# Kernel optimization log

Measured on AMD Instinct MI355X. Metric: run time of the kernel, lower is better.

## Reference

```python
import jax, jax.numpy as jnp
import numpy as np

N = 10000
E = 80000
NUM_TYPES = 1000
IN_CH = 64
EMB = 128
IN_GNN = EMB + IN_CH - 1  # 191
NUM_GRAPHS = 16
NUM_CLASSES = 2


def _glorot(key, shape):
    fan_in, fan_out = shape[0], shape[1]
    lim = jnp.sqrt(6.0 / (fan_in + fan_out))
    return jax.random.uniform(key, shape, jnp.float32, -lim, lim)


def setup_inputs() -> dict:
    key = jax.random.key(0)
    ks = jax.random.split(key, 20)
    node_type_ids = jax.random.randint(ks[0], (N,), 0, NUM_TYPES)
    other_feats = jax.random.normal(ks[1], (N, IN_CH - 1), jnp.float32)
    edge_index = jax.random.randint(ks[2], (2, E), 0, N)
    batch = jnp.sort(jax.random.randint(ks[3], (N,), 0, NUM_GRAPHS))
    params = dict(
        emb=jax.random.normal(ks[4], (NUM_TYPES, EMB), jnp.float32),
        W1=_glorot(ks[5], (IN_GNN, 2048)), b1=jnp.zeros((2048,), jnp.float32),
        W2=_glorot(ks[6], (2048, 1024)), b2=jnp.zeros((1024,), jnp.float32),
        W3=_glorot(ks[7], (1024, 1024)), b3=jnp.zeros((1024,), jnp.float32),
        h1w=_glorot(ks[8], (1024, 1024)), h1b=jnp.zeros((1024,), jnp.float32),
        h2w=_glorot(ks[9], (1024, 1024)), h2b=jnp.zeros((1024,), jnp.float32),
        h3w=_glorot(ks[10], (1024, 512)), h3b=jnp.zeros((512,), jnp.float32),
        ow=_glorot(ks[11], (512, NUM_CLASSES)), ob=jnp.zeros((NUM_CLASSES,), jnp.float32),
    )
    return dict(node_type_ids=node_type_ids, other_feats=other_feats,
                edge_index=edge_index, batch=batch, **params)


def _gcn_norm(edge_index, num_nodes):
    # add self loops + symmetric normalization D^-1/2 (A+I) D^-1/2 (PyG GCNConv defaults)
    loop = jnp.arange(num_nodes, dtype=edge_index.dtype)
    src = jnp.concatenate([edge_index[0], loop])
    dst = jnp.concatenate([edge_index[1], loop])
    deg = jax.ops.segment_sum(jnp.ones_like(src, jnp.float32), dst, num_segments=num_nodes)
    dinv = jnp.where(deg > 0, jax.lax.rsqrt(jnp.maximum(deg, 1.0)), 0.0)
    norm = dinv[src] * dinv[dst]
    return src, dst, norm


def _gcn_conv(x, src, dst, norm, W, b):
    h = x @ W                                    # [N, out] dense GEMM first (PyG order)
    msg = h[src] * norm[:, None]                 # gather + scale over edges
    agg = jax.ops.segment_sum(msg, dst, num_segments=x.shape[0])  # scatter-add
    return agg + b


def reference(node_type_ids, other_feats, edge_index, batch,
              emb, W1, b1, W2, b2, W3, b3,
              h1w, h1b, h2w, h2b, h3w, h3b, ow, ob):
    # eval mode: dropout is identity
    x = jnp.concatenate([emb[node_type_ids], other_feats], axis=-1)  # [N, 191]
    src, dst, norm = _gcn_norm(edge_index, x.shape[0])
    x = jax.nn.relu(_gcn_conv(x, src, dst, norm, W1, b1))
    x = jax.nn.relu(_gcn_conv(x, src, dst, norm, W2, b2))
    x = jax.nn.relu(_gcn_conv(x, src, dst, norm, W3, b3))
    # global mean pool over graphs
    sums = jax.ops.segment_sum(x, batch, num_segments=NUM_GRAPHS)
    cnts = jax.ops.segment_sum(jnp.ones((x.shape[0],), jnp.float32), batch, num_segments=NUM_GRAPHS)
    g = sums / jnp.maximum(cnts, 1.0)[:, None]   # [G, 1024]
    g = jax.nn.relu(g @ h1w + h1b)
    g = jax.nn.relu(g @ h2w + h2b)
    g = jax.nn.relu(g @ h3w + h3b)
    return g @ ow + ob                           # [G, num_classes]
```

## Files before the change

### kernel.cpp

```cpp
#include <hip/hip_runtime.h>


#define N_NODES 10000
#define N_EDGES 80000
#define EMB_DIM 128
#define FEAT_DIM 63
#define IN_GNN 191
#define IN_STRIDE 192
#define H1 2048
#define H2 1024
#define NGRAPH 16
#define NCLS 2
#define PCHUNK 8

#define GLB_AS __attribute__((address_space(1)))
#define LDS_AS __attribute__((address_space(3)))

using ushort = unsigned short;
typedef __attribute__((ext_vector_type(8))) short s8b;
typedef __attribute__((ext_vector_type(4))) float f4v;

__device__ __forceinline__ float us2f(ushort u) {
    union { unsigned int i; float f; } v; v.i = ((unsigned int)u) << 16; return v.f;
}
__device__ __forceinline__ ushort f2us(float f) {
    union { unsigned int i; float f; } v; v.f = f;
    unsigned int r = v.i + 0x7FFFu + ((v.i >> 16) & 1u);
    return (ushort)(r >> 16);
}
__device__ __forceinline__ float ldm(const void* p, long i, int md) {
    return (md == 1) ? us2f(((const ushort*)p)[i]) : ((const float*)p)[i];
}
__device__ __forceinline__ void gl_lds16(const ushort* g, ushort* l) {
    __builtin_amdgcn_global_load_lds((const GLB_AS unsigned int*)g,
                                     (LDS_AS unsigned int*)l, 16, 0, 0);
}

__global__ void GraphV1EmbLarge_73864847556672_kernel() {}

__global__ void k_detect(const ushort* __restrict__ feats, int* __restrict__ mode) {
    if (threadIdx.x != 0 || blockIdx.x != 0) return;
    int sane = 0;
    for (int i = 0; i < 256; i++) {
        ushort u = feats[i];
        int e = (u >> 7) & 0xFF;
        if (u == 0 || (e >= 97 && e <= 157)) sane++;
    }
    *mode = (sane >= 220) ? 1 : 2;
}

__global__ void k_zero2(int* __restrict__ a, int na, float* __restrict__ b, int nb) {
    int i = blockIdx.x * 256 + threadIdx.x;
    if (i < na) a[i] = 0;
    if (i < nb) b[i] = 0.f;
}
__global__ void k_deg_i(const int* __restrict__ dst, int* __restrict__ cnt) {
    int e = blockIdx.x * blockDim.x + threadIdx.x;
    if (e < N_EDGES) atomicAdd(&cnt[dst[e]], 1);
}
__global__ void k_dinv_i(const int* __restrict__ cnt, float* __restrict__ dinv) {
    int i = blockIdx.x * blockDim.x + threadIdx.x;
    if (i < N_NODES) dinv[i] = rsqrtf((float)cnt[i] + 1.0f);
}
__global__ void k_scan(const int* __restrict__ cnt, int* __restrict__ indptr) {
    __shared__ int part[256];
    int t = threadIdx.x;
    int base = t * 40;
    int s = 0;
    for (int i = 0; i < 40; i++) { int idx = base + i; if (idx < N_NODES) s += cnt[idx]; }
    part[t] = s;
    __syncthreads();
    if (t == 0) {
        int run = 0;
        for (int i = 0; i < 256; i++) { int tmp = part[i]; part[i] = run; run += tmp; }
        indptr[N_NODES] = run;
    }
    __syncthreads();
    int run = part[t];
    for (int i = 0; i < 40; i++) {
        int idx = base + i;
        if (idx < N_NODES) { indptr[idx] = run; run += cnt[idx]; }
    }
}
__global__ void k_fill(const int* __restrict__ src, const int* __restrict__ dst,
                       const int* __restrict__ indptr, int* __restrict__ cursor,
                       const float* __restrict__ dinv, int* __restrict__ ecol,
                       float* __restrict__ ewgt) {
    int e = blockIdx.x * blockDim.x + threadIdx.x;
    if (e >= N_EDGES) return;
    int d = dst[e], s = src[e];
    int slot = indptr[d] + atomicAdd(&cursor[d], 1);
    ecol[slot] = s;
    ewgt[slot] = dinv[s] * dinv[d];
}
__global__ void k_starts(const int* __restrict__ batch, int* __restrict__ starts) {
    int i = blockIdx.x * blockDim.x + threadIdx.x;
    if (i > N_NODES) return;
    int bc = (i < N_NODES) ? batch[i] : NGRAPH;
    int bp = (i == 0) ? -1 : batch[i - 1];
    for (int g = bp + 1; g <= bc; g++) starts[g] = i;
}

__global__ void k_build_x0(const int* __restrict__ types, const void* __restrict__ emb,
                           const void* __restrict__ feats, ushort* __restrict__ x0,
                           const int* __restrict__ mode) {
    int md = *mode;
    int i = blockIdx.x;
    int c = threadIdx.x;
    float v = 0.f;
    if (c < EMB_DIM) v = ldm(emb, (long)types[i] * EMB_DIM + c, md);
    else if (c < IN_GNN) v = ldm(feats, (long)i * FEAT_DIM + (c - EMB_DIM), md);
    x0[(long)i * IN_STRIDE + c] = f2us(v);
}

__global__ void k_cvtT(const void* __restrict__ W, int K, int N, int Kp,
                       ushort* __restrict__ Wt, const int* __restrict__ mode) {
    __shared__ float tile[32][33];
    int md = *mode;
    int n0 = blockIdx.x * 32, k0 = blockIdx.y * 32;
    int tx = threadIdx.x, ty = threadIdx.y;
    for (int r = ty; r < 32; r += 8) {
        int k = k0 + r;
        tile[r][tx] = (k < K) ? ldm(W, (long)k * N + n0 + tx, md) : 0.f;
    }
    __syncthreads();
    for (int r = ty; r < 32; r += 8) {
        int nn = n0 + r, kk = k0 + tx;
        if (kk < Kp) Wt[(long)nn * Kp + kk] = f2us(tile[tx][r]);
    }
}

__global__ void k_biases(const void* __restrict__ b1, const void* __restrict__ b2,
                         const void* __restrict__ b3, float* __restrict__ b1f,
                         float* __restrict__ b2f, float* __restrict__ b3f,
                         const int* __restrict__ mode) {
    int md = *mode;
    int i = blockIdx.x * 256 + threadIdx.x;
    if (i < 2048) b1f[i] = ldm(b1, i, md);
    else if (i < 3072) b2f[i - 2048] = ldm(b2, (long)(i - 2048), md);
    else if (i < 4096) b3f[i - 3072] = ldm(b3, (long)(i - 3072), md);
}

__global__ void k_gather192(const ushort* __restrict__ H, const int* __restrict__ indptr,
                            const int* __restrict__ ecol, const float* __restrict__ ewgt,
                            const float* __restrict__ dinv, ushort* __restrict__ X) {
    int d = blockIdx.x;
    int c = threadIdx.x;
    float ds = dinv[d];
    float acc = us2f(H[(long)d * IN_STRIDE + c]) * ds * ds;
    int s0 = indptr[d], s1 = indptr[d + 1];
    for (int s = s0; s < s1; s++) {
        int sc = ecol[s];
        float w = ewgt[s];
        acc += us2f(H[(long)sc * IN_STRIDE + c]) * w;
    }
    X[(long)d * IN_STRIDE + c] = f2us(acc);
}

__device__ __forceinline__ void unpack8(uint4 u, float* f) {
    f[0] = us2f((ushort)(u.x & 0xffff)); f[1] = us2f((ushort)(u.x >> 16));
    f[2] = us2f((ushort)(u.y & 0xffff)); f[3] = us2f((ushort)(u.y >> 16));
    f[4] = us2f((ushort)(u.z & 0xffff)); f[5] = us2f((ushort)(u.z >> 16));
    f[6] = us2f((ushort)(u.w & 0xffff)); f[7] = us2f((ushort)(u.w >> 16));
}

__global__ void k_gather1024(const ushort* __restrict__ H, const int* __restrict__ indptr,
                             const int* __restrict__ ecol, const float* __restrict__ ewgt,
                             const float* __restrict__ dinv, const float* __restrict__ bias,
                             ushort* __restrict__ X) {
    int d = blockIdx.x;
    int c8 = threadIdx.x * 8;
    float ds = dinv[d];
    float a[8], f[8];
    unpack8(*(const uint4*)&H[(long)d * H2 + c8], a);
    float w0 = ds * ds;
#pragma unroll
    for (int r = 0; r < 8; r++) a[r] *= w0;
    int s0 = indptr[d], s1 = indptr[d + 1];
    for (int s = s0; s < s1; s++) {
        int sc = ecol[s];
        float w = ewgt[s];
        unpack8(*(const uint4*)&H[(long)sc * H2 + c8], f);
#pragma unroll
        for (int r = 0; r < 8; r++) a[r] += f[r] * w;
    }
    uint4 o;
    unsigned int p0 = (unsigned int)f2us(fmaxf(a[0] + bias[c8 + 0], 0.f));
    unsigned int p1 = (unsigned int)f2us(fmaxf(a[1] + bias[c8 + 1], 0.f));
    unsigned int p2 = (unsigned int)f2us(fmaxf(a[2] + bias[c8 + 2], 0.f));
    unsigned int p3 = (unsigned int)f2us(fmaxf(a[3] + bias[c8 + 3], 0.f));
    unsigned int p4 = (unsigned int)f2us(fmaxf(a[4] + bias[c8 + 4], 0.f));
    unsigned int p5 = (unsigned int)f2us(fmaxf(a[5] + bias[c8 + 5], 0.f));
    unsigned int p6 = (unsigned int)f2us(fmaxf(a[6] + bias[c8 + 6], 0.f));
    unsigned int p7 = (unsigned int)f2us(fmaxf(a[7] + bias[c8 + 7], 0.f));
    o.x = p0 | (p1 << 16); o.y = p2 | (p3 << 16);
    o.z = p4 | (p5 << 16); o.w = p6 | (p7 << 16);
    *(uint4*)&X[(long)d * H2 + c8] = o;
}

__global__ __launch_bounds__(256) void k_mfma_gemm(
    const ushort* __restrict__ A, int lda, int M,
    const ushort* __restrict__ Wt, int K, int N,
    const float* __restrict__ bias, int relu,
    ushort* __restrict__ C) {
    __shared__ ushort As[128 * 32];
    __shared__ ushort Bs[128 * 32];
    int n0 = blockIdx.x * 128, m0 = blockIdx.y * 128;
    int tid = threadIdx.x;
    int wave = tid >> 6, lane = tid & 63;
    int wm = (wave & 1) * 64, wn = (wave >> 1) * 64;
    int quad = lane >> 4, l16 = lane & 15;

    int rr = lane >> 2;
    int cc = (lane & 3) * 8;
    int rA0 = wave * 16 + rr, rA1 = 64 + rA0;
    int gmA0 = m0 + rA0; if (gmA0 >= M) gmA0 = M - 1;
    int gmA1 = m0 + rA1; if (gmA1 >= M) gmA1 = M - 1;
    const ushort* aS0 = A + (long)gmA0 * lda + cc;
    const ushort* aS1 = A + (long)gmA1 * lda + cc;
    const ushort* bS0 = Wt + (long)(n0 + rA0) * K + cc;
    const ushort* bS1 = Wt + (long)(n0 + rA1) * K + cc;
    ushort* aD0 = As + wave * 512;
    ushort* aD1 = As + 2048 + wave * 512;
    ushort* bD0 = Bs + wave * 512;
    ushort* bD1 = Bs + 2048 + wave * 512;

    f4v acc[4][4];
#pragma unroll
    for (int i = 0; i < 4; i++)
#pragma unroll
        for (int j = 0; j < 4; j++) acc[i][j] = (f4v)(0.f);

    for (int k0 = 0; k0 < K; k0 += 32) {
        gl_lds16(aS0, aD0);
        gl_lds16(aS1, aD1);
        gl_lds16(bS0, bD0);
        gl_lds16(bS1, bD1);
        aS0 += 32; aS1 += 32; bS0 += 32; bS1 += 32;
        __syncthreads();
        s8b a[4], b[4];
#pragma unroll
        for (int i = 0; i < 4; i++)
            a[i] = *(const s8b*)&As[(wm + i * 16 + l16) * 32 + quad * 8];
#pragma unroll
        for (int j = 0; j < 4; j++)
            b[j] = *(const s8b*)&Bs[(wn + j * 16 + l16) * 32 + quad * 8];
#pragma unroll
        for (int i = 0; i < 4; i++)
#pragma unroll
            for (int j = 0; j < 4; j++)
                acc[i][j] = __builtin_amdgcn_mfma_f32_16x16x32_bf16(a[i], b[j], acc[i][j], 0, 0, 0);
        __syncthreads();
    }

#pragma unroll
    for (int i = 0; i < 4; i++) {
        int row0 = m0 + wm + i * 16 + quad * 4;
#pragma unroll
        for (int j = 0; j < 4; j++) {
            int colc = n0 + wn + j * 16 + l16;
            float bv = bias ? bias[colc] : 0.f;
#pragma unroll
            for (int r = 0; r < 4; r++) {
                int row = row0 + r;
                if (row < M) {
                    float v = acc[i][j][r] + bv;
                    if (relu) v = fmaxf(v, 0.f);
                    C[(long)row * N + colc] = f2us(v);
                }
            }
        }
    }
}

__global__ void k_pool_part(const ushort* __restrict__ x, const int* __restrict__ starts,
                            float* __restrict__ acc) {
    int g = blockIdx.x / PCHUNK, ch = blockIdx.x % PCHUNK;
    int c = blockIdx.y * 256 + threadIdx.x;
    int s0 = starts[g], s1 = starts[g + 1];
    int len = s1 - s0;
    int per = (len + PCHUNK - 1) / PCHUNK;
    int r0 = s0 + ch * per;
    int r1 = r0 + per; if (r1 > s1) r1 = s1;
    if (r0 >= r1) return;
    float sum = 0.f;
    for (int i = r0; i < r1; i++) sum += us2f(x[(long)i * H2 + c]);
    atomicAdd(&acc[g * H2 + c], sum);
}
__global__ void k_pool_fin(const float* __restrict__ acc, const int* __restrict__ starts,
                           ushort* __restrict__ pA) {
    int idx = blockIdx.x * 256 + threadIdx.x;
    if (idx >= NGRAPH * H2) return;
    int g = idx >> 10;
    int cnt = starts[g + 1] - starts[g];
    pA[idx] = f2us(acc[idx] / (float)(cnt > 0 ? cnt : 1));
}

__global__ __launch_bounds__(256) void k_head_mfma(const ushort* __restrict__ A,
                                                   const ushort* __restrict__ Wt,
                                                   float* __restrict__ pt, int N) {
    __shared__ float red[4][16][16];
    int n0 = blockIdx.x * 16;
    int ks = blockIdx.y;
    int wave = threadIdx.x >> 6, lane = threadIdx.x & 63;
    int l16 = lane & 15, quad = lane >> 4;
    int kbase = ks * 256 + wave * 64;
    f4v acc = (f4v)(0.f);
#pragma unroll
    for (int kk = 0; kk < 64; kk += 32) {
        int k = kbase + kk + quad * 8;
        s8b a = *(const s8b*)&A[l16 * 1024 + k];
        s8b b = *(const s8b*)&Wt[(long)(n0 + l16) * 1024 + k];
        acc = __builtin_amdgcn_mfma_f32_16x16x32_bf16(a, b, acc, 0, 0, 0);
    }
#pragma unroll
    for (int r = 0; r < 4; r++) red[wave][quad * 4 + r][l16] = acc[r];
    __syncthreads();
    int row = threadIdx.x >> 4, col = threadIdx.x & 15;
    float s = red[0][row][col] + red[1][row][col] + red[2][row][col] + red[3][row][col];
    pt[((long)ks * 16 + row) * N + n0 + col] = s;
}

__global__ void k_head_red(const float* __restrict__ pt, const void* __restrict__ bias,
                           ushort* __restrict__ out, int N,
                           const int* __restrict__ mode) {
    int md = *mode;
    int idx = blockIdx.x * 256 + threadIdx.x;
    if (idx >= 16 * N) return;
    int row = idx / N, col = idx - row * N;
    float s = pt[((long)0 * 16 + row) * N + col] + pt[((long)1 * 16 + row) * N + col]
            + pt[((long)2 * 16 + row) * N + col] + pt[((long)3 * 16 + row) * N + col];
    s = fmaxf(s + ldm(bias, (long)col, md), 0.f);
    out[(long)row * N + col] = f2us(s);
}

__global__ void k_head_out(const ushort* __restrict__ in, const void* __restrict__ W,
                           const void* __restrict__ b, void* __restrict__ out,
                           const int* __restrict__ mode) {
    int md = *mode;
    int row = blockIdx.x >> 1, cls = blockIdx.x & 1;
    int lane = threadIdx.x;
    float acc = 0.f;
    for (int k = lane; k < 512; k += 64)
        acc += us2f(in[row * 512 + k]) * ldm(W, (long)k * NCLS + cls, md);
#pragma unroll
    for (int off = 32; off > 0; off >>= 1) acc += __shfl_down(acc, off);
    if (lane == 0) {
        float v = acc + ldm(b, (long)cls, md);
        if (md == 1) ((ushort*)out)[row * NCLS + cls] = f2us(v);
        else ((float*)out)[row * NCLS + cls] = v;
    }
}

extern "C" void kernel_launch(void* const* d_in, const int* in_sizes, int n_in,
                              void* d_out, int out_size, void* d_ws, size_t ws_size,
                              hipStream_t stream) {
    static const int EXPECT[19] = {
        10000, 630000, 160000, 10000, 128000,
        391168, 2048, 2097152, 1024, 1048576, 1024,
        1048576, 1024, 1048576, 1024, 524288, 512, 1024, 2
    };
    if (n_in != 19) { hipMemsetAsync(d_out, 0x48, 64, stream); return; }
    for (int i = 0; i < 19; i++)
        if (in_sizes[i] != EXPECT[i]) { hipMemsetAsync(d_out, 0x50 + i, 64, stream); return; }
    if (ws_size < (size_t)90000000) { hipMemsetAsync(d_out, 0x49, 64, stream); return; }

    const int* node_types = (const int*)d_in[0];
    const void* other = d_in[1];
    const int* e_src = (const int*)d_in[2];
    const int* e_dst = e_src + N_EDGES;
    const int* batch = (const int*)d_in[3];

    char* w = (char*)d_ws;
    int* mode = (int*)w;      w += 256;
    int* cnt = (int*)w;       w += 10240 * 4;
    int* cursor = (int*)w;    w += 10240 * 4;
    float* dinv = (float*)w;  w += 10240 * 4;
    int* starts = (int*)w;    w += 256;
    int* indptr = (int*)w;    w += 10240 * 4;
    int* ecol = (int*)w;      w += 81920 * 4;
    float* ewgt = (float*)w;  w += 81920 * 4;
    float* b1f = (float*)w;   w += 2048 * 4;
    float* b2f = (float*)w;   w += 1024 * 4;
    float* b3f = (float*)w;   w += 1024 * 4;
    float* pt = (float*)w;    w += 4 * 16 * 1024 * 4;
    float* pacc = (float*)w;  w += 16 * 1024 * 4;
    ushort* pA = (ushort*)w;  w += 16 * 1024 * 2;
    ushort* hA = (ushort*)w;  w += 16 * 1024 * 2;
    ushort* hB = (ushort*)w;  w += 16 * 1024 * 2;
    ushort* x0 = (ushort*)w;  w += 1920000 * 2;
    ushort* A1 = (ushort*)w;  w += 1920000 * 2;
    ushort* W1t = (ushort*)w; w += 393216 * 2;
    ushort* W2t = (ushort*)w; w += 2097152 * 2;
    ushort* W3t = (ushort*)w; w += 1048576 * 2;
    ushort* h1wt = (ushort*)w; w += 1048576 * 2;
    ushort* h2wt = (ushort*)w; w += 1048576 * 2;
    ushort* h3wt = (ushort*)w; w += 524288 * 2;
    ushort* Hb = (ushort*)w;  w += 20480000 * 2;
    ushort* Gb = (ushort*)w;  w += 10240000 * 2;
    ushort* x2 = Hb;
    ushort* x3 = Hb + (size_t)N_NODES * H2;

    hipGetLastError();
    k_detect<<<1, 64, 0, stream>>>((const ushort*)other, mode);
    hipError_t e0 = hipGetLastError();
    if (e0 != hipSuccess) { hipMemsetAsync(d_out, 0x46, 64, stream); return; }

    k_zero2<<<80, 256, 0, stream>>>(cnt, 20480, pacc, NGRAPH * H2);
    k_deg_i<<<(N_EDGES + 255) / 256, 256, 0, stream>>>(e_dst, cnt);
    k_dinv_i<<<(N_NODES + 255) / 256, 256, 0, stream>>>(cnt, dinv);
    k_starts<<<(N_NODES + 256) / 256, 256, 0, stream>>>(batch, starts);
    k_scan<<<1, 256, 0, stream>>>(cnt, indptr);
    k_fill<<<(N_EDGES + 255) / 256, 256, 0, stream>>>(e_src, e_dst, indptr, cursor, dinv, ecol, ewgt);

    k_build_x0<<<N_NODES, IN_STRIDE, 0, stream>>>(node_types, d_in[4], other, x0, mode);
    k_cvtT<<<dim3(H1 / 32, IN_STRIDE / 32), dim3(32, 8), 0, stream>>>(d_in[5], IN_GNN, H1, IN_STRIDE, W1t, mode);
    k_cvtT<<<dim3(H2 / 32, H1 / 32), dim3(32, 8), 0, stream>>>(d_in[7], H1, H2, H1, W2t, mode);
    k_cvtT<<<dim3(H2 / 32, H2 / 32), dim3(32, 8), 0, stream>>>(d_in[9], H2, H2, H2, W3t, mode);
    k_cvtT<<<dim3(H2 / 32, H2 / 32), dim3(32, 8), 0, stream>>>(d_in[11], H2, H2, H2, h1wt, mode);
    k_cvtT<<<dim3(H2 / 32, H2 / 32), dim3(32, 8), 0, stream>>>(d_in[13], H2, H2, H2, h2wt, mode);
    k_cvtT<<<dim3(512 / 32, H2 / 32), dim3(32, 8), 0, stream>>>(d_in[15], H2, 512, H2, h3wt, mode);
    k_biases<<<16, 256, 0, stream>>>(d_in[6], d_in[8], d_in[10], b1f, b2f, b3f, mode);

    const int MB = (N_NODES + 127) / 128;

    k_gather192<<<N_NODES, IN_STRIDE, 0, stream>>>(x0, indptr, ecol, ewgt, dinv, A1);
    k_mfma_gemm<<<dim3(H1 / 128, MB), 256, 0, stream>>>(A1, IN_STRIDE, N_NODES, W1t, IN_STRIDE, H1, b1f, 1, Hb);

    k_mfma_gemm<<<dim3(H2 / 128, MB), 256, 0, stream>>>(Hb, H1, N_NODES, W2t, H1, H2, nullptr, 0, Gb);
    k_gather1024<<<N_NODES, 128, 0, stream>>>(Gb, indptr, ecol, ewgt, dinv, b2f, x2);

    k_mfma_gemm<<<dim3(H2 / 128, MB), 256, 0, stream>>>(x2, H2, N_NODES, W3t, H2, H2, nullptr, 0, Gb);
    k_gather1024<<<N_NODES, 128, 0, stream>>>(Gb, indptr, ecol, ewgt, dinv, b3f, x3);

    k_pool_part<<<dim3(NGRAPH * PCHUNK, H2 / 256), 256, 0, stream>>>(x3, starts, pacc);
    k_pool_fin<<<64, 256, 0, stream>>>(pacc, starts, pA);

    k_head_mfma<<<dim3(64, 4), 256, 0, stream>>>(pA, h1wt, pt, 1024);
    k_head_red<<<64, 256, 0, stream>>>(pt, d_in[12], hA, 1024, mode);
    k_head_mfma<<<dim3(64, 4), 256, 0, stream>>>(hA, h2wt, pt, 1024);
    k_head_red<<<64, 256, 0, stream>>>(pt, d_in[14], hB, 1024, mode);
    k_head_mfma<<<dim3(32, 4), 256, 0, stream>>>(hB, h3wt, pt, 512);
    k_head_red<<<32, 256, 0, stream>>>(pt, d_in[16], hA, 512, mode);
    k_head_out<<<NGRAPH * NCLS, 64, 0, stream>>>(hA, d_in[17], d_in[18], d_out, mode);

    hipError_t e1 = hipGetLastError();
    if (e1 != hipSuccess) hipMemsetAsync(d_out, 0x47, 64, stream);
}
```

Measured before the change: 451.4 us.

## Rework GEMM staging with padded LDS, grouped tile order, and fused prep kernels

Replaces the direct global-to-LDS loads in the MFMA GEMM with register-staged vector loads into padded LDS tiles (row pitch 40) to reduce bank conflicts. The grid becomes 1D with a grouped M/N tile swizzle so that eight M-tiles share weight tiles for better L2 reuse. It also folds the dinv computation into the scan kernel and merges the six weight transpose-convert launches into one kernel, cutting launch overhead. The register-staged path adds a global-load latency stall before each barrier, since there is no double buffering.

```diff
diff --git a/kernel.cpp b/kernel.cpp
--- a/kernel.cpp
+++ b/kernel.cpp
@@ -12,9 +12,7 @@
 #define NGRAPH 16
 #define NCLS 2
 #define PCHUNK 8
-
-#define GLB_AS __attribute__((address_space(1)))
-#define LDS_AS __attribute__((address_space(3)))
+#define LDP 40
 
 using ushort = unsigned short;
 typedef __attribute__((ext_vector_type(8))) short s8b;
@@ -30,10 +28,6 @@
 }
 __device__ __forceinline__ float ldm(const void* p, long i, int md) {
     return (md == 1) ? us2f(((const ushort*)p)[i]) : ((const float*)p)[i];
-}
-__device__ __forceinline__ void gl_lds16(const ushort* g, ushort* l) {
-    __builtin_amdgcn_global_load_lds((const GLB_AS unsigned int*)g,
-                                     (LDS_AS unsigned int*)l, 16, 0, 0);
 }
 
 __global__ void GraphV1EmbLarge_73864847556672_kernel() {}
@@ -58,11 +52,8 @@
     int e = blockIdx.x * blockDim.x + threadIdx.x;
     if (e < N_EDGES) atomicAdd(&cnt[dst[e]], 1);
 }
-__global__ void k_dinv_i(const int* __restrict__ cnt, float* __restrict__ dinv) {
-    int i = blockIdx.x * blockDim.x + threadIdx.x;
-    if (i < N_NODES) dinv[i] = rsqrtf((float)cnt[i] + 1.0f);
-}
-__global__ void k_scan(const int* __restrict__ cnt, int* __restrict__ indptr) {
+__global__ void k_scan(const int* __restrict__ cnt, int* __restrict__ indptr,
+                       float* __restrict__ dinv) {
     __shared__ int part[256];
     int t = threadIdx.x;
     int base = t * 40;
@@ -79,7 +70,10 @@
     int run = part[t];
     for (int i = 0; i < 40; i++) {
         int idx = base + i;
-        if (idx < N_NODES) { indptr[idx] = run; run += cnt[idx]; }
+        if (idx < N_NODES) {
+            indptr[idx] = run; run += cnt[idx];
+            dinv[idx] = rsqrtf((float)cnt[idx] + 1.0f);
+        }
     }
 }
 __global__ void k_fill(const int* __restrict__ src, const int* __restrict__ dst,
@@ -113,11 +107,9 @@
     x0[(long)i * IN_STRIDE + c] = f2us(v);
 }
 
-__global__ void k_cvtT(const void* __restrict__ W, int K, int N, int Kp,
-                       ushort* __restrict__ Wt, const int* __restrict__ mode) {
+__device__ __forceinline__ void cvt_tile(const void* W, int K, int N, int Kp,
+                                         ushort* Wt, int n0, int k0, int md) {
     __shared__ float tile[32][33];
-    int md = *mode;
-    int n0 = blockIdx.x * 32, k0 = blockIdx.y * 32;
     int tx = threadIdx.x, ty = threadIdx.y;
     for (int r = ty; r < 32; r += 8) {
         int k = k0 + r;
@@ -127,6 +119,28 @@
     for (int r = ty; r < 32; r += 8) {
         int nn = n0 + r, kk = k0 + tx;
         if (kk < Kp) Wt[(long)nn * Kp + kk] = f2us(tile[tx][r]);
+    }
+}
+
+__global__ void k_cvtT_all(const void* W1, const void* W2, const void* W3,
+                           const void* h1, const void* h2, const void* h3,
+                           ushort* W1t, ushort* W2t, ushort* W3t,
+                           ushort* h1t, ushort* h2t, ushort* h3t,
+                           const int* __restrict__ mode) {
+    int md = *mode;
+    int b = blockIdx.x;
+    if (b < 384) {
+        int t = b;        cvt_tile(W1, IN_GNN, H1, IN_STRIDE, W1t, (t % 64) * 32, (t / 64) * 32, md);
+    } else if (b < 2432) {
+        int t = b - 384;  cvt_tile(W2, H1, H2, H1, W2t, (t % 32) * 32, (t / 32) * 32, md);
+    } else if (b < 3456) {
+        int t = b - 2432; cvt_tile(W3, H2, H2, H2, W3t, (t % 32) * 32, (t / 32) * 32, md);
+    } else if (b < 4480) {
+        int t = b - 3456; cvt_tile(h1, H2, H2, H2, h1t, (t % 32) * 32, (t / 32) * 32, md);
+    } else if (b < 5504) {
+        int t = b - 4480; cvt_tile(h2, H2, H2, H2, h2t, (t % 32) * 32, (t / 32) * 32, md);
+    } else {
+        int t = b - 5504; cvt_tile(h3, H2, 512, H2, h3t, (t % 16) * 32, (t / 16) * 32, md);
     }
 }
 
@@ -202,69 +216,73 @@
     const ushort* __restrict__ A, int lda, int M,
     const ushort* __restrict__ Wt, int K, int N,
     const float* __restrict__ bias, int relu,
-    ushort* __restrict__ C) {
-    __shared__ ushort As[128 * 32];
-    __shared__ ushort Bs[128 * 32];
-    int n0 = blockIdx.x * 128, m0 = blockIdx.y * 128;
+    ushort* __restrict__ C, int NB) {
+    __shared__ ushort As[128 * LDP];
+    __shared__ ushort Bs[128 * LDP];
+    int L = blockIdx.x;
+    int i = L >> 3;
+    int m_t = (L & 7) + (i / NB) * 8;
+    int n_t = i % NB;
+    int m0 = m_t * 128, n0 = n_t * 128;
+    if (m0 >= M) return;
     int tid = threadIdx.x;
     int wave = tid >> 6, lane = tid & 63;
     int wm = (wave & 1) * 64, wn = (wave >> 1) * 64;
     int quad = lane >> 4, l16 = lane & 15;
-
-    int rr = lane >> 2;
-    int cc = (lane & 3) * 8;
-    int rA0 = wave * 16 + rr, rA1 = 64 + rA0;
-    int gmA0 = m0 + rA0; if (gmA0 >= M) gmA0 = M - 1;
-    int gmA1 = m0 + rA1; if (gmA1 >= M) gmA1 = M - 1;
-    const ushort* aS0 = A + (long)gmA0 * lda + cc;
-    const ushort* aS1 = A + (long)gmA1 * lda + cc;
-    const ushort* bS0 = Wt + (long)(n0 + rA0) * K + cc;
-    const ushort* bS1 = Wt + (long)(n0 + rA1) * K + cc;
-    ushort* aD0 = As + wave * 512;
-    ushort* aD1 = As + 2048 + wave * 512;
-    ushort* bD0 = Bs + wave * 512;
-    ushort* bD1 = Bs + 2048 + wave * 512;
+    int srow = tid >> 2;
+    int scol = (tid & 3) * 8;
 
     f4v acc[4][4];
 #pragma unroll
-    for (int i = 0; i < 4; i++)
-#pragma unroll
-        for (int j = 0; j < 4; j++) acc[i][j] = (f4v)(0.f);
+    for (int ii = 0; ii < 4; ii++)
+#pragma unroll
+        for (int jj = 0; jj < 4; jj++) acc[ii][jj] = (f4v)(0.f);
+
+    int gm1 = m0 + srow;       if (gm1 >= M) gm1 = M - 1;
+    int gm2 = m0 + 64 + srow;  if (gm2 >= M) gm2 = M - 1;
+    const ushort* pa1 = A + (long)gm1 * lda + scol;
+    const ushort* pa2 = A + (long)gm2 * lda + scol;
+    const ushort* pb1 = Wt + (long)(n0 + srow) * K + scol;
+    const ushort* pb2 = Wt + (long)(n0 + 64 + srow) * K + scol;
 
     for (int k0 = 0; k0 < K; k0 += 32) {
-        gl_lds16(aS0, aD0);
-        gl_lds16(aS1, aD1);
-        gl_lds16(bS0, bD0);
-        gl_lds16(bS1, bD1);
-        aS0 += 32; aS1 += 32; bS0 += 32; bS1 += 32;
+        s8b va1 = *(const s8b*)pa1;
+        s8b va2 = *(const s8b*)pa2;
+        s8b vb1 = *(const s8b*)pb1;
+        s8b vb2 = *(const s8b*)pb2;
+        pa1 += 32; pa2 += 32; pb1 += 32; pb2 += 32;
+        __syncthreads();
+        *(s8b*)&As[srow * LDP + scol] = va1;
+        *(s8b*)&As[(64 + srow) * LDP + scol] = va2;
+        *(s8b*)&Bs[srow * LDP + scol] = vb1;
+        *(s8b*)&Bs[(64 + srow) * LDP + scol] = vb2;
         __syncthreads();
         s8b a[4], b[4];
 #pragma unroll
-        for (int i = 0; i < 4; i++)
-            a[i] = *(const s8b*)&As[(wm + i * 16 + l16) * 32 + quad * 8];
-#pragma unroll
-        for (int j = 0; j < 4; j++)
-            b[j] = *(const s8b*)&Bs[(wn + j * 16 + l16) * 32 + quad * 8];
-#pragma unroll
-        for (int i = 0; i < 4; i++)
-#pragma unroll
-            for (int j = 0; j < 4; j++)
-                acc[i][j] = __builtin_amdgcn_mfma_f32_16x16x32_bf16(a[i], b[j], acc[i][j], 0, 0, 0);
-        __syncthreads();
-    }
-
-#pragma unroll
-    for (int i = 0; i < 4; i++) {
-        int row0 = m0 + wm + i * 16 + quad * 4;
-#pragma unroll
-        for (int j = 0; j < 4; j++) {
-            int colc = n0 + wn + j * 16 + l16;
+        for (int ii = 0; ii < 4; ii++)
+            a[ii] = *(const s8b*)&As[(wm + ii * 16 + l16) * LDP + quad * 8];
+#pragma unroll
+        for (int jj = 0; jj < 4; jj++)
+            b[jj] = *(const s8b*)&Bs[(wn + jj * 16 + l16) * LDP + quad * 8];
+#pragma unroll
+        for (int ii = 0; ii < 4; ii++)
+#pragma unroll
+            for (int jj = 0; jj < 4; jj++)
+                acc[ii][jj] = __builtin_amdgcn_mfma_f32_16x16x32_bf16(a[ii], b[jj], acc[ii][jj], 0, 0, 0);
+    }
+
+#pragma unroll
+    for (int ii = 0; ii < 4; ii++) {
+        int row0 = m0 + wm + ii * 16 + quad * 4;
+#pragma unroll
+        for (int jj = 0; jj < 4; jj++) {
+            int colc = n0 + wn + jj * 16 + l16;
             float bv = bias ? bias[colc] : 0.f;
 #pragma unroll
             for (int r = 0; r < 4; r++) {
                 int row = row0 + r;
                 if (row < M) {
-                    float v = acc[i][j][r] + bv;
+                    float v = acc[ii][jj][r] + bv;
                     if (relu) v = fmaxf(v, 0.f);
                     C[(long)row * N + colc] = f2us(v);
                 }
@@ -408,29 +426,22 @@
 
     k_zero2<<<80, 256, 0, stream>>>(cnt, 20480, pacc, NGRAPH * H2);
     k_deg_i<<<(N_EDGES + 255) / 256, 256, 0, stream>>>(e_dst, cnt);
-    k_dinv_i<<<(N_NODES + 255) / 256, 256, 0, stream>>>(cnt, dinv);
     k_starts<<<(N_NODES + 256) / 256, 256, 0, stream>>>(batch, starts);
-    k_scan<<<1, 256, 0, stream>>>(cnt, indptr);
+    k_scan<<<1, 256, 0, stream>>>(cnt, indptr, dinv);
     k_fill<<<(N_EDGES + 255) / 256, 256, 0, stream>>>(e_src, e_dst, indptr, cursor, dinv, ecol, ewgt);
 
     k_build_x0<<<N_NODES, IN_STRIDE, 0, stream>>>(node_types, d_in[4], other, x0, mode);
-    k_cvtT<<<dim3(H1 / 32, IN_STRIDE / 32), dim3(32, 8), 0, stream>>>(d_in[5], IN_GNN, H1, IN_STRIDE, W1t, mode);
-    k_cvtT<<<dim3(H2 / 32, H1 / 32), dim3(32, 8), 0, stream>>>(d_in[7], H1, H2, H1, W2t, mode);
-    k_cvtT<<<dim3(H2 / 32, H2 / 32), dim3(32, 8), 0, stream>>>(d_in[9], H2, H2, H2, W3t, mode);
-    k_cvtT<<<dim3(H2 / 32, H2 / 32), dim3(32, 8), 0, stream>>>(d_in[11], H2, H2, H2, h1wt, mode);
-    k_cvtT<<<dim3(H2 / 32, H2 / 32), dim3(32, 8), 0, stream>>>(d_in[13], H2, H2, H2, h2wt, mode);
-    k_cvtT<<<dim3(512 / 32, H2 / 32), dim3(32, 8), 0, stream>>>(d_in[15], H2, 512, H2, h3wt, mode);
+    k_cvtT_all<<<6016, dim3(32, 8), 0, stream>>>(d_in[5], d_in[7], d_in[9], d_in[11], d_in[13], d_in[15],
+                                                 W1t, W2t, W3t, h1wt, h2wt, h3wt, mode);
     k_biases<<<16, 256, 0, stream>>>(d_in[6], d_in[8], d_in[10], b1f, b2f, b3f, mode);
 
-    const int MB = (N_NODES + 127) / 128;
-
     k_gather192<<<N_NODES, IN_STRIDE, 0, stream>>>(x0, indptr, ecol, ewgt, dinv, A1);
-    k_mfma_gemm<<<dim3(H1 / 128, MB), 256, 0, stream>>>(A1, IN_STRIDE, N_NODES, W1t, IN_STRIDE, H1, b1f, 1, Hb);
-
-    k_mfma_gemm<<<dim3(H2 / 128, MB), 256, 0, stream>>>(Hb, H1, N_NODES, W2t, H1, H2, nullptr, 0, Gb);
+    k_mfma_gemm<<<16 * 80, 256, 0, stream>>>(A1, IN_STRIDE, N_NODES, W1t, IN_STRIDE, H1, b1f, 1, Hb, 16);
+
+    k_mfma_gemm<<<8 * 80, 256, 0, stream>>>(Hb, H1, N_NODES, W2t, H1, H2, nullptr, 0, Gb, 8);
     k_gather1024<<<N_NODES, 128, 0, stream>>>(Gb, indptr, ecol, ewgt, dinv, b2f, x2);
 
-    k_mfma_gemm<<<dim3(H2 / 128, MB), 256, 0, stream>>>(x2, H2, N_NODES, W3t, H2, H2, nullptr, 0, Gb);
+    k_mfma_gemm<<<8 * 80, 256, 0, stream>>>(x2, H2, N_NODES, W3t, H2, H2, nullptr, 0, Gb, 8);
     k_gather1024<<<N_NODES, 128, 0, stream>>>(Gb, indptr, ecol, ewgt, dinv, b3f, x3);
 
     k_pool_part<<<dim3(NGRAPH * PCHUNK, H2 / 256), 256, 0, stream>>>(x3, starts, pacc);
```

After: 433.1 us. 1.04x faster.
